# Kernel optimization log

Measured on AMD Instinct MI355X. Metric: run time of the kernel, lower is better.

Reference implementation:

```python
import jax, jax.numpy as jnp
import numpy as np

B, C, M, N = 8, 256, 4, 2048
CK = C // M  # k_conv input channels
EPS_BN = 1e-5


def setup_inputs() -> dict:
    key = jax.random.key(0)
    ks = jax.random.split(key, 10)
    s = 0.05
    return {
        "q": jax.random.normal(ks[0], (B, C, N), jnp.float32),
        "x": jax.random.normal(ks[1], (B, CK, N), jnp.float32),
        "Wq": jax.random.normal(ks[2], (C, C), jnp.float32) * s,   # q_conv (no bias)
        "Wk": jax.random.normal(ks[3], (C, CK), jnp.float32) * s,  # k_conv (no bias)
        "Wv": jax.random.normal(ks[4], (C, C), jnp.float32) * s,   # v_conv
        "bv": jax.random.normal(ks[5], (C,), jnp.float32) * s,
        "Wt": jax.random.normal(ks[6], (C, C), jnp.float32) * s,   # trans_conv
        "bt": jax.random.normal(ks[7], (C,), jnp.float32) * s,
        "gamma": jnp.ones((C,), jnp.float32),                      # BatchNorm1d weight
        "beta": jnp.zeros((C,), jnp.float32),                      # BatchNorm1d bias
    }


def reference(q, x, Wq, Wk, Wv, bv, Wt, bt, gamma, beta):
    # 1x1 Conv1d == per-point channel matmul
    x_q = jnp.einsum("oc,bcn->bno", Wq, q)                  # [B, N, C]
    x_k = jnp.einsum("oc,bcn->bon", Wk, x)                  # [B, C, N]
    x_v = jnp.einsum("oc,bcn->bon", Wv, q) + bv[None, :, None]  # [B, C, N]

    energy = jnp.einsum("bnc,bcm->bnm", x_q, x_k)           # [B, Nq, Nk]
    attention = jax.nn.softmax(energy, axis=-1)
    # extra L1 renormalization over the query dimension (dim=1)
    attention = attention / (1e-9 + attention.sum(axis=1, keepdims=True))

    x_r = jnp.einsum("bcn,bnm->bcm", x_v, attention)        # [B, C, Nk]

    y = jnp.einsum("oc,bcn->bon", Wt, x_r) + bt[None, :, None]
    # BatchNorm1d in training mode: batch statistics over (B, N) per channel
    mean = y.mean(axis=(0, 2), keepdims=True)
    var = ((y - mean) ** 2).mean(axis=(0, 2), keepdims=True)
    y = (y - mean) * jax.lax.rsqrt(var + EPS_BN)
    y = y * gamma[None, :, None] + beta[None, :, None]
    return jax.nn.relu(y)
```

## Files before the change

kernel.cpp:

```cpp
#include <hip/hip_runtime.h>
#include <hip/hip_bf16.h>

#define NB  8
#define NC  256
#define NCK 64
#define SEQ 2048

typedef unsigned short u16;
typedef short bfrag8 __attribute__((ext_vector_type(8)));
typedef float ffrag4 __attribute__((ext_vector_type(4)));

#define MFMA16(a, b, c) __builtin_amdgcn_mfma_f32_16x16x32_bf16((a), (b), (c), 0, 0, 0)

static __device__ __forceinline__ u16 f2bf(float f) {
  return __builtin_bit_cast(u16, (__bf16)f);
}
static __device__ __forceinline__ float bf2f(u16 u) {
  unsigned v = (unsigned)u << 16;
  return __builtin_bit_cast(float, v);
}

__global__ __launch_bounds__(256) void wconv_kernel(
    const float* __restrict__ Wv, const float* __restrict__ Wt,
    u16* __restrict__ dst, float* __restrict__ zz, float* __restrict__ rowsum_g) {
  int bx = blockIdx.x;
  if (bx >= 512) {
    if (bx == 512) {
      zz[threadIdx.x] = 0.f;
      zz[256 + threadIdx.x] = 0.f;
    } else {
      rowsum_g[(bx - 513) * 256 + threadIdx.x] = 0.f;
    }
    return;
  }
  int id = bx * 256 + threadIdx.x;
  const float* src;
  int off;
  if (id < 65536) { src = Wv; off = 131072; }
  else            { src = Wt; off = 262144; id -= 65536; }
  float v = src[id];
  u16 h = f2bf(v);
  u16 l = f2bf(v - bf2f(h));
  dst[off + id] = h;
  dst[off + 65536 + id] = l;
}

template <int CIN>
__global__ __launch_bounds__(256) void tconv_kernel(
    const float* __restrict__ in, u16* __restrict__ Thi, u16* __restrict__ Tlo) {
  __shared__ float t[32][33];
  const int tid = threadIdx.x;
  const int b = blockIdx.x & 7, cg = blockIdx.x >> 3;
  const int c0 = cg << 5, n0 = blockIdx.y << 5;
  {
    int c = tid >> 3, m4 = (tid & 7) << 2;
    float4 v = *(const float4*)&in[((size_t)b * CIN + c0 + c) * SEQ + n0 + m4];
    t[c][m4 + 0] = v.x; t[c][m4 + 1] = v.y; t[c][m4 + 2] = v.z; t[c][m4 + 3] = v.w;
  }
  __syncthreads();
  {
    int n = tid >> 3, c4 = (tid & 7) << 2;
    u16 h[4], l[4];
#pragma unroll
    for (int j = 0; j < 4; ++j) {
      float v = t[c4 + j][n];
      h[j] = f2bf(v);
      l[j] = f2bf(v - bf2f(h[j]));
    }
    size_t base = ((size_t)b * SEQ + n0 + n) * CIN + c0 + c4;
    *(uint2*)&Thi[base] = make_uint2((unsigned)h[0] | ((unsigned)h[1] << 16),
                                     (unsigned)h[2] | ((unsigned)h[3] << 16));
    *(uint2*)&Tlo[base] = make_uint2((unsigned)l[0] | ((unsigned)l[1] << 16),
                                     (unsigned)l[2] | ((unsigned)l[3] << 16));
  }
}

__global__ __launch_bounds__(256) void gcomp_kernel(
    const float* __restrict__ Wq, const float* __restrict__ Wk,
    u16* __restrict__ Gh, u16* __restrict__ Gl) {
  const int ck = blockIdx.x, c = threadIdx.x;
  float s = 0.f;
#pragma unroll 8
  for (int o = 0; o < 256; ++o) s += Wq[o * 256 + c] * Wk[o * 64 + ck];
  u16 h = f2bf(s);
  Gh[ck * 256 + c] = h;
  Gl[ck * 256 + c] = f2bf(s - bf2f(h));
}

template <int K, bool WA>
__global__ __launch_bounds__(256, 2) void gemm_kernel(
    const u16* __restrict__ Ahi, const u16* __restrict__ Alo,
    const u16* __restrict__ Whi, const u16* __restrict__ Wlo,
    const float* __restrict__ bias, u16* __restrict__ outp) {
  constexpr int SP = K + 8;
  extern __shared__ u16 lds[];
  const int tid = threadIdx.x;
  const int wv = tid >> 6, lane = tid & 63, quad = lane >> 4, ln = lane & 15;
  const int b = blockIdx.x & 7, nt = blockIdx.x >> 3;
  const int o0 = blockIdx.y << 6, n0 = nt << 7;

  constexpr int RW = K / 8;
  for (int i = tid; i < 64 * RW; i += 256) {
    int row = i / RW, kc = (i % RW) * 8;
    *(uint4*)&lds[row * SP + kc] = *(const uint4*)&Whi[(size_t)(o0 + row) * K + kc];
    *(uint4*)&lds[(64 + row) * SP + kc] = *(const uint4*)&Wlo[(size_t)(o0 + row) * K + kc];
  }
  constexpr int NA = K / 32;
  bfrag8 ahi[2][NA], alo[2][NA];
#pragma unroll
  for (int rs = 0; rs < 2; ++rs) {
    const u16* ap = Ahi + ((size_t)b * SEQ + n0 + wv * 32 + rs * 16 + ln) * K + quad * 8;
    const u16* al = Alo + ((size_t)b * SEQ + n0 + wv * 32 + rs * 16 + ln) * K + quad * 8;
#pragma unroll
    for (int a = 0; a < NA; ++a) {
      ahi[rs][a] = *(const bfrag8*)(ap + a * 32);
      alo[rs][a] = *(const bfrag8*)(al + a * 32);
    }
  }
  __syncthreads();

  ffrag4 acc[2][4];
#pragma unroll
  for (int ot = 0; ot < 4; ++ot) {
    ffrag4 e0 = {0.f, 0.f, 0.f, 0.f}, e1 = {0.f, 0.f, 0.f, 0.f};
#pragma unroll
    for (int a = 0; a < NA; ++a) {
      bfrag8 wh = *(const bfrag8*)&lds[(ot * 16 + ln) * SP + a * 32 + quad * 8];
      bfrag8 wl = *(const bfrag8*)&lds[(64 + ot * 16 + ln) * SP + a * 32 + quad * 8];
      if (WA) {
        e0 = MFMA16(wh, ahi[0][a], e0);
        e0 = MFMA16(wh, alo[0][a], e0);
        e0 = MFMA16(wl, ahi[0][a], e0);
        e1 = MFMA16(wh, ahi[1][a], e1);
        e1 = MFMA16(wh, alo[1][a], e1);
        e1 = MFMA16(wl, ahi[1][a], e1);
      } else {
        e0 = MFMA16(ahi[0][a], wh, e0);
        e0 = MFMA16(alo[0][a], wh, e0);
        e0 = MFMA16(ahi[0][a], wl, e0);
        e1 = MFMA16(ahi[1][a], wh, e1);
        e1 = MFMA16(alo[1][a], wh, e1);
        e1 = MFMA16(ahi[1][a], wl, e1);
      }
    }
    acc[0][ot] = e0;
    acc[1][ot] = e1;
  }
  __syncthreads();

  if (!WA) {
    u16* tl = lds;
#pragma unroll
    for (int rs = 0; rs < 2; ++rs)
#pragma unroll
      for (int ot = 0; ot < 4; ++ot)
#pragma unroll
        for (int r = 0; r < 4; ++r)
          tl[(wv * 32 + rs * 16 + quad * 4 + r) * 72 + ot * 16 + ln] = f2bf(acc[rs][ot][r]);
    __syncthreads();
    for (int i = tid; i < 128 * 8; i += 256) {
      int row = i >> 3, c8 = (i & 7) * 8;
      *(uint4*)&outp[((size_t)b * SEQ + n0 + row) * NC + o0 + c8] = *(uint4*)&tl[row * 72 + c8];
    }
  } else {
    u16* tl = lds;
#pragma unroll
    for (int rs = 0; rs < 2; ++rs)
#pragma unroll
      for (int ot = 0; ot < 4; ++ot)
#pragma unroll
        for (int r = 0; r < 4; ++r)
          tl[(ot * 16 + quad * 4 + r) * 136 + wv * 32 + rs * 16 + ln] = f2bf(acc[rs][ot][r]);
    __syncthreads();
    for (int i = tid; i < 64 * 16; i += 256) {
      int row = i >> 4, n8 = (i & 15) * 8;
      float bb = (bias != nullptr) ? bias[o0 + row] : 0.f;
      u16 pk[8];
#pragma unroll
      for (int j = 0; j < 8; ++j) pk[j] = f2bf(bf2f(tl[row * 136 + n8 + j]) + bb);
      *(uint4*)&outp[((size_t)b * NC + o0 + row) * SEQ + n0 + n8] = *(uint4*)pk;
    }
  }
}

__global__ __launch_bounds__(256, 2) void gemmxg_kernel(
    const u16* __restrict__ Ahi, const u16* __restrict__ Alo,
    const u16* __restrict__ Gh, const u16* __restrict__ Gl,
    u16* __restrict__ xg) {
  constexpr int K = 256, SP = K + 8;
  __shared__ u16 lds[128 * SP];
  const int tid = threadIdx.x;
  const int wv = tid >> 6, lane = tid & 63, quad = lane >> 4, ln = lane & 15;
  const int b = blockIdx.x & 7, nt = blockIdx.x >> 3;
  const int n0 = nt << 7;

  for (int i = tid; i < 64 * 32; i += 256) {
    int row = i >> 5, kc = (i & 31) * 8;
    *(uint4*)&lds[row * SP + kc] = *(const uint4*)&Gh[(size_t)row * K + kc];
    *(uint4*)&lds[(64 + row) * SP + kc] = *(const uint4*)&Gl[(size_t)row * K + kc];
  }
  bfrag8 ahi[2][8], alo[2][8];
#pragma unroll
  for (int rs = 0; rs < 2; ++rs) {
    const u16* ap = Ahi + ((size_t)b * SEQ + n0 + wv * 32 + rs * 16 + ln) * K + quad * 8;
    const u16* al = Alo + ((size_t)b * SEQ + n0 + wv * 32 + rs * 16 + ln) * K + quad * 8;
#pragma unroll
    for (int a = 0; a < 8; ++a) {
      ahi[rs][a] = *(const bfrag8*)(ap + a * 32);
      alo[rs][a] = *(const bfrag8*)(al + a * 32);
    }
  }
  __syncthreads();

  ffrag4 acc[2][4];
#pragma unroll
  for (int ot = 0; ot < 4; ++ot) {
    ffrag4 e0 = {0.f, 0.f, 0.f, 0.f}, e1 = {0.f, 0.f, 0.f, 0.f};
#pragma unroll
    for (int a = 0; a < 8; ++a) {
      bfrag8 wh = *(const bfrag8*)&lds[(ot * 16 + ln) * SP + a * 32 + quad * 8];
      bfrag8 wl = *(const bfrag8*)&lds[(64 + ot * 16 + ln) * SP + a * 32 + quad * 8];
      e0 = MFMA16(ahi[0][a], wh, e0);
      e0 = MFMA16(alo[0][a], wh, e0);
      e0 = MFMA16(ahi[0][a], wl, e0);
      e1 = MFMA16(ahi[1][a], wh, e1);
      e1 = MFMA16(alo[1][a], wh, e1);
      e1 = MFMA16(ahi[1][a], wl, e1);
    }
    acc[0][ot] = e0;
    acc[1][ot] = e1;
  }
  __syncthreads();

  u16* tl = lds;
#pragma unroll
  for (int rs = 0; rs < 2; ++rs)
#pragma unroll
    for (int ot = 0; ot < 4; ++ot)
#pragma unroll
      for (int r = 0; r < 4; ++r)
        tl[(wv * 32 + rs * 16 + quad * 4 + r) * 72 + ot * 16 + ln] = f2bf(acc[rs][ot][r]);
  __syncthreads();
  for (int i = tid; i < 128 * 8; i += 256) {
    int row = i >> 3, c8 = (i & 7) * 8;
    *(uint4*)&xg[((size_t)b * SEQ + n0 + row) * NCK + c8] = *(uint4*)&tl[row * 72 + c8];
  }
}

__global__ __launch_bounds__(256, 2) void rowsum_kernel(
    const u16* __restrict__ xg, const u16* __restrict__ xTh,
    const u16* __restrict__ xTl, float* __restrict__ rowsum_g) {
  __shared__ u16 bk_l[2][2][64 * 76];
  const int tid = threadIdx.x;
  const int wv = tid >> 6, lane = tid & 63, quad = lane >> 4, ln = lane & 15;
  const int b  = blockIdx.x & 7;
  const int nt = (blockIdx.x >> 3) & 15;
  const int mh = blockIdx.x >> 7;
  const int n0 = nt << 7;
  const int m0 = mh << 9;

  bfrag8 aq[2][2];
#pragma unroll
  for (int rs = 0; rs < 2; ++rs) {
    const u16* qp = xg + ((size_t)b * SEQ + n0 + wv * 32 + rs * 16 + ln) * NCK + quad * 8;
    aq[rs][0] = *(const bfrag8*)qp;
    aq[rs][1] = *(const bfrag8*)(qp + 32);
  }

  const int srow = tid >> 2, scol = (tid & 3) << 4;
  uint4 ph0, ph1, pl0, pl1;
  {
    size_t base = ((size_t)b * SEQ + m0 + srow) * NCK + scol;
    ph0 = *(const uint4*)&xTh[base];     ph1 = *(const uint4*)&xTh[base + 8];
    pl0 = *(const uint4*)&xTl[base];     pl1 = *(const uint4*)&xTl[base + 8];
  }

  float rsum[2][4];
#pragma unroll
  for (int rs = 0; rs < 2; ++rs)
#pragma unroll
    for (int r = 0; r < 4; ++r) rsum[rs][r] = 0.f;

  for (int ch = 0; ch < 8; ++ch) {
    u16* bh = &bk_l[ch & 1][0][srow * 76 + scol];
    u16* bl = &bk_l[ch & 1][1][srow * 76 + scol];
    *(uint4*)bh = ph0; *(uint4*)(bh + 8) = ph1;
    *(uint4*)bl = pl0; *(uint4*)(bl + 8) = pl1;
    if (ch < 7) {
      size_t base = ((size_t)b * SEQ + m0 + (ch + 1) * 64 + srow) * NCK + scol;
      ph0 = *(const uint4*)&xTh[base];   ph1 = *(const uint4*)&xTh[base + 8];
      pl0 = *(const uint4*)&xTl[base];   pl1 = *(const uint4*)&xTl[base + 8];
    }
    __syncthreads();

    ffrag4 e[2][4];
#pragma unroll
    for (int rs = 0; rs < 2; ++rs)
#pragma unroll
      for (int ms = 0; ms < 4; ++ms) e[rs][ms] = (ffrag4){0.f, 0.f, 0.f, 0.f};
#pragma unroll
    for (int ms = 0; ms < 4; ++ms)
#pragma unroll
      for (int kk = 0; kk < 2; ++kk) {
        bfrag8 bbh = *(const bfrag8*)&bk_l[ch & 1][0][(ms * 16 + ln) * 76 + kk * 32 + quad * 8];
        bfrag8 bbl = *(const bfrag8*)&bk_l[ch & 1][1][(ms * 16 + ln) * 76 + kk * 32 + quad * 8];
        e[0][ms] = MFMA16(aq[0][kk], bbh, e[0][ms]);
        e[0][ms] = MFMA16(aq[0][kk], bbl, e[0][ms]);
        e[1][ms] = MFMA16(aq[1][kk], bbh, e[1][ms]);
        e[1][ms] = MFMA16(aq[1][kk], bbl, e[1][ms]);
      }
#pragma unroll
    for (int rs = 0; rs < 2; ++rs)
#pragma unroll
      for (int ms = 0; ms < 4; ++ms)
#pragma unroll
        for (int r = 0; r < 4; ++r) rsum[rs][r] += __expf(e[rs][ms][r]);
  }

#pragma unroll
  for (int msk = 1; msk < 16; msk <<= 1)
#pragma unroll
    for (int rs = 0; rs < 2; ++rs)
#pragma unroll
      for (int r = 0; r < 4; ++r) rsum[rs][r] += __shfl_xor(rsum[rs][r], msk, 64);
  if (ln == 0) {
#pragma unroll
    for (int rs = 0; rs < 2; ++rs)
#pragma unroll
      for (int r = 0; r < 4; ++r)
        atomicAdd(&rowsum_g[(size_t)b * SEQ + n0 + wv * 32 + rs * 16 + quad * 4 + r],
                  rsum[rs][r]);
  }
}

__global__ __launch_bounds__(512, 4) void attn_kernel(
    const u16* __restrict__ xg, const u16* __restrict__ xTh,
    const u16* __restrict__ xTl, const u16* __restrict__ xv,
    const float* __restrict__ rowsum_g,
    u16* __restrict__ U, float* __restrict__ csum) {
  __shared__ u16 xg_l[32 * 76];
  __shared__ u16 p_l[64 * 40];
  __shared__ float ri_l[32];
  __shared__ float cs_l[64];
  const int tid = threadIdx.x;
  const int wv = tid >> 6, lane = tid & 63, quad = lane >> 4, ln = lane & 15;
  const int b = blockIdx.x & 7;
  const int m0 = ((blockIdx.x >> 3) & 31) << 6;
  const int half = blockIdx.x >> 8;
  const int nsub = wv & 1, msub = wv >> 1;
  const int nt0 = half * 32, ntEnd = nt0 + 32;

  if (tid < 64) cs_l[tid] = 0.f;

  bfrag8 bkh[2], bkl[2];
  {
    size_t base = ((size_t)b * SEQ + m0 + msub * 16 + ln) * NCK + quad * 8;
#pragma unroll
    for (int kk = 0; kk < 2; ++kk) {
      bkh[kk] = *(const bfrag8*)&xTh[base + kk * 32];
      bkl[kk] = *(const bfrag8*)&xTl[base + kk * 32];
    }
  }

  const int prow = (tid & 255) >> 3, pcol = (tid & 7) << 3;
  uint4 pf0 = {0, 0, 0, 0};
  float rspf = 1.f;
  bfrag8 avpf0, avpf1;
  {
    const int n0 = nt0 << 5;
    if (tid < 256) pf0 = *(const uint4*)&xg[((size_t)b * SEQ + n0 + prow) * NCK + pcol];
    if (tid < 32) rspf = rowsum_g[(size_t)b * SEQ + n0 + tid];
    const u16* vp = &xv[((size_t)b * NC + wv * 32 + ln) * SEQ + n0 + quad * 8];
    avpf0 = *(const bfrag8*)vp;
    avpf1 = *(const bfrag8*)(vp + 16 * SEQ);
  }

  ffrag4 acc[2][4];
#pragma unroll
  for (int ct = 0; ct < 2; ++ct)
#pragma unroll
    for (int s = 0; s < 4; ++s) acc[ct][s] = (ffrag4){0.f, 0.f, 0.f, 0.f};
  float cs = 0.f;

  for (int nt = nt0; nt < ntEnd; ++nt) {
    bfrag8 av0 = avpf0, av1 = avpf1;
    if (tid < 256) *(uint4*)&xg_l[prow * 76 + pcol] = pf0;
    if (tid < 32) ri_l[tid] = 1.0f / rspf;
    {
      const int ntn = (nt + 1 < ntEnd) ? nt + 1 : nt;
      const int n0n = ntn << 5;
      if (tid < 256) pf0 = *(const uint4*)&xg[((size_t)b * SEQ + n0n + prow) * NCK + pcol];
      if (tid < 32) rspf = rowsum_g[(size_t)b * SEQ + n0n + tid];
      const u16* vp = &xv[((size_t)b * NC + wv * 32 + ln) * SEQ + n0n + quad * 8];
      avpf0 = *(const bfrag8*)vp;
      avpf1 = *(const bfrag8*)(vp + 16 * SEQ);
    }
    __syncthreads();
    {
      ffrag4 e = {0.f, 0.f, 0.f, 0.f};
#pragma unroll
      for (int kk = 0; kk < 2; ++kk) {
        bfrag8 a = *(const bfrag8*)&xg_l[(nsub * 16 + ln) * 76 + kk * 32 + quad * 8];
        e = MFMA16(a, bkh[kk], e);
        e = MFMA16(a, bkl[kk], e);
      }
      u16 pu[4];
#pragma unroll
      for (int r = 0; r < 4; ++r) {
        float p = __expf(e[r]) * ri_l[nsub * 16 + quad * 4 + r];
        cs += p;
        pu[r] = f2bf(p);
      }
      *(uint2*)&p_l[(msub * 16 + ln) * 40 + nsub * 16 + quad * 4] =
          make_uint2((unsigned)pu[0] | ((unsigned)pu[1] << 16),
                     (unsigned)pu[2] | ((unsigned)pu[3] << 16));
    }
    __syncthreads();
#pragma unroll
    for (int s = 0; s < 4; ++s) {
      bfrag8 pb = *(const bfrag8*)&p_l[(s * 16 + ln) * 40 + quad * 8];
      acc[0][s] = MFMA16(av0, pb, acc[0][s]);
      acc[1][s] = MFMA16(av1, pb, acc[1][s]);
    }
  }

  cs += __shfl_down(cs, 32, 64);
  cs += __shfl_down(cs, 16, 64);
  if (lane < 16) atomicAdd(&cs_l[msub * 16 + ln], cs);
  __syncthreads();
  if (tid < 64) csum[((size_t)half * NB + b) * SEQ + m0 + tid] = cs_l[tid];

  u16* Uh = U + (size_t)half * NB * SEQ * NC;
#pragma unroll
  for (int ct = 0; ct < 2; ++ct)
#pragma unroll
    for (int s = 0; s < 4; ++s) {
      u16 pk[4];
#pragma unroll
      for (int r = 0; r < 4; ++r) pk[r] = f2bf(acc[ct][s][r]);
      *(uint2*)&Uh[((size_t)b * SEQ + m0 + s * 16 + ln) * NC + wv * 32 + ct * 16 + quad * 4] =
          make_uint2((unsigned)pk[0] | ((unsigned)pk[1] << 16),
                     (unsigned)pk[2] | ((unsigned)pk[3] << 16));
    }
}

__global__ __launch_bounds__(256, 2) void gemmt_kernel(
    const u16* __restrict__ U, const float* __restrict__ csum,
    const u16* __restrict__ Whi, const u16* __restrict__ Wlo,
    const float* __restrict__ bias, float* __restrict__ outp,
    float* __restrict__ ssum, float* __restrict__ sqsum) {
  constexpr int K = NC, SP = K + 8;
  __shared__ u16 lds[128 * SP];
  __shared__ float bsum[64], bsq[64];
  const int tid = threadIdx.x;
  const int wv = tid >> 6, lane = tid & 63, quad = lane >> 4, ln = lane & 15;
  const int b = blockIdx.x & 7, nt = blockIdx.x >> 3;
  const int o0 = blockIdx.y << 6, n0 = nt << 7;
  const size_t SZu = (size_t)NB * SEQ * NC;

  if (tid < 64) { bsum[tid] = 0.f; bsq[tid] = 0.f; }

  for (int i = tid; i < 64 * 32; i += 256) {
    int row = i >> 5, kc = (i & 31) * 8;
    *(uint4*)&lds[row * SP + kc] = *(const uint4*)&Whi[(size_t)(o0 + row) * K + kc];
    *(uint4*)&lds[(64 + row) * SP + kc] = *(const uint4*)&Wlo[(size_t)(o0 + row) * K + kc];
  }

  bfrag8 af[2][8];
#pragma unroll
  for (int rs = 0; rs < 2; ++rs) {
    const int row = n0 + wv * 32 + rs * 16 + ln;
    const float ic = 1.0f / (1e-9f + csum[(size_t)b * SEQ + row] +
                             csum[((size_t)NB + b) * SEQ + row]);
    const u16* up = U + ((size_t)b * SEQ + row) * NC + quad * 8;
#pragma unroll
    for (int a = 0; a < 8; ++a) {
      bfrag8 u0 = *(const bfrag8*)(up + a * 32);
      bfrag8 u1 = *(const bfrag8*)(up + SZu + a * 32);
      union { u16 u[8]; bfrag8 f; } t;
#pragma unroll
      for (int j = 0; j < 8; ++j)
        t.u[j] = f2bf((bf2f((u16)u0[j]) + bf2f((u16)u1[j])) * ic);
      af[rs][a] = t.f;
    }
  }
  __syncthreads();

  ffrag4 acc[2][4];
#pragma unroll
  for (int ot = 0; ot < 4; ++ot) {
    ffrag4 e0 = {0.f, 0.f, 0.f, 0.f}, e1 = {0.f, 0.f, 0.f, 0.f};
#pragma unroll
    for (int a = 0; a < 8; ++a) {
      bfrag8 wh = *(const bfrag8*)&lds[(ot * 16 + ln) * SP + a * 32 + quad * 8];
      bfrag8 wl = *(const bfrag8*)&lds[(64 + ot * 16 + ln) * SP + a * 32 + quad * 8];
      e0 = MFMA16(wh, af[0][a], e0);
      e0 = MFMA16(wl, af[0][a], e0);
      e1 = MFMA16(wh, af[1][a], e1);
      e1 = MFMA16(wl, af[1][a], e1);
    }
    acc[0][ot] = e0;
    acc[1][ot] = e1;
  }
  __syncthreads();

  float* fl = (float*)lds;
#pragma unroll
  for (int rs = 0; rs < 2; ++rs)
#pragma unroll
    for (int ot = 0; ot < 4; ++ot)
#pragma unroll
      for (int r = 0; r < 4; ++r)
        fl[(ot * 16 + quad * 4 + r) * 132 + wv * 32 + rs * 16 + ln] = acc[rs][ot][r];
  __syncthreads();
  for (int i = tid; i < 64 * 32; i += 256) {
    int row = i >> 5, n4 = (i & 31) * 4;
    float bb = (bias != nullptr) ? bias[o0 + row] : 0.f;
    const float* src = &fl[row * 132 + n4];
    float4 v = *(const float4*)src;
    v.x += bb; v.y += bb; v.z += bb; v.w += bb;
    *(float4*)&outp[((size_t)b * NC + o0 + row) * SEQ + n0 + n4] = v;
    float s = v.x + v.y + v.z + v.w;
    float sq = v.x * v.x + v.y * v.y + v.z * v.z + v.w * v.w;
    atomicAdd(&bsum[row], s);
    atomicAdd(&bsq[row], sq);
  }
  __syncthreads();
  if (tid < 64) {
    atomicAdd(&ssum[o0 + tid], bsum[tid]);
    atomicAdd(&sqsum[o0 + tid], bsq[tid]);
  }
}

__global__ __launch_bounds__(256) void bnorm_kernel(
    const float* __restrict__ y, const float* __restrict__ ssum, const float* __restrict__ sqsum,
    const float* __restrict__ gamma, const float* __restrict__ beta, float* __restrict__ out) {
  size_t e0 = ((size_t)blockIdx.x * 256 + threadIdx.x) * 4;
  int o = (int)((e0 >> 11) & (NC - 1));
  const float invn = 1.0f / 16384.0f;
  float mean = ssum[o] * invn;
  float var = sqsum[o] * invn - mean * mean;
  float rs = rsqrtf(var + 1e-5f);
  float a = gamma[o] * rs;
  float c = beta[o] - mean * a;
  float4 v = *(const float4*)(y + e0);
  float4 r;
  r.x = fmaxf(0.f, fmaf(v.x, a, c));
  r.y = fmaxf(0.f, fmaf(v.y, a, c));
  r.z = fmaxf(0.f, fmaf(v.z, a, c));
  r.w = fmaxf(0.f, fmaf(v.w, a, c));
  *(float4*)(out + e0) = r;
}

extern "C" void kernel_launch(void* const* d_in, const int* in_sizes, int n_in,
                              void* d_out, int out_size, void* d_ws, size_t ws_size,
                              hipStream_t stream) {
  const float* q     = (const float*)d_in[0];
  const float* x     = (const float*)d_in[1];
  const float* Wq    = (const float*)d_in[2];
  const float* Wk    = (const float*)d_in[3];
  const float* Wv    = (const float*)d_in[4];
  const float* bv    = (const float*)d_in[5];
  const float* Wt    = (const float*)d_in[6];
  const float* bt    = (const float*)d_in[7];
  const float* gamma = (const float*)d_in[8];
  const float* beta  = (const float*)d_in[9];
  float* out = (float*)d_out;

  const size_t SZ = (size_t)NB * NC * SEQ;
  const size_t SZB = SZ * 4;
  char* wsb = (char*)d_ws;
  u16* qT_hi = (u16*)(wsb);
  u16* qT_lo = qT_hi + SZ;
  u16* U     = (u16*)(wsb);
  float* y   = (float*)(wsb + 2 * SZB);
  u16* xv    = (u16*)(wsb + 3 * SZB);
  u16* wpack = (u16*)(wsb + 3 * SZB + SZB / 2);
  u16* Wv_hi = wpack + 131072, *Wv_lo = wpack + 196608;
  u16* Wt_hi = wpack + 262144, *Wt_lo = wpack + 327680;
  float* rowsum_g = (float*)(wpack + 425984);
  float* csum = rowsum_g + (size_t)NB * SEQ;
  float* ssum = csum + 2 * (size_t)NB * SEQ;
  float* sqsum = ssum + NC;
  u16* xT_hi = (u16*)(wsb + ((size_t)64 << 20));
  u16* xT_lo = (u16*)(wsb + ((size_t)66 << 20));
  u16* xg    = (u16*)(wsb + ((size_t)72 << 20));
  u16* Gp_hi = (u16*)(wsb + ((size_t)78 << 20));
  u16* Gp_lo = Gp_hi + 64 * 256;

  wconv_kernel<<<577, 256, 0, stream>>>(Wv, Wt, wpack, ssum, rowsum_g);
  tconv_kernel<NC><<<dim3(64, 64), 256, 0, stream>>>(q, qT_hi, qT_lo);
  tconv_kernel<NCK><<<dim3(16, 64), 256, 0, stream>>>(x, xT_hi, xT_lo);
  gcomp_kernel<<<64, 256, 0, stream>>>(Wq, Wk, Gp_hi, Gp_lo);

  const size_t shm256 = 64 * (256 + 8) * 2 * sizeof(u16);
  gemm_kernel<256, true><<<dim3(128, 4), 256, shm256, stream>>>(
      qT_hi, qT_lo, Wv_hi, Wv_lo, bv, xv);
  gemmxg_kernel<<<128, 256, 0, stream>>>(qT_hi, qT_lo, Gp_hi, Gp_lo, xg);

  rowsum_kernel<<<512, 256, 0, stream>>>(xg, xT_hi, xT_lo, rowsum_g);
  attn_kernel<<<512, 512, 0, stream>>>(xg, xT_hi, xT_lo, xv, rowsum_g, U, csum);
  gemmt_kernel<<<dim3(128, 4), 256, 0, stream>>>(
      U, csum, Wt_hi, Wt_lo, bt, y, ssum, sqsum);

  bnorm_kernel<<<4096, 256, 0, stream>>>(y, ssum, sqsum, gamma, beta, out);
}
```

Measured before the change: 224.2 us.

## Split attention and rowsum over more blocks, load fragments directly from global

The rowsum and attention kernels are split four ways along their reduction dimension instead of two, doubling the grid to 1024 blocks. Attention partials now go to two U buffers with four csum slices that the Wt GEMM sums. Both kernels drop the LDS staging of xg and key tiles and load MFMA fragments straight from global memory. Attention double-buffers the probability tile so each iteration needs one barrier instead of two. This targets low occupancy and barrier overhead, at the cost of writing and reading twice as much partial-U traffic in the GEMM.

```diff
diff --git a/kernel.cpp b/kernel.cpp
--- a/kernel.cpp
+++ b/kernel.cpp
@@ -250,14 +250,13 @@
 __global__ __launch_bounds__(256, 2) void rowsum_kernel(
     const u16* __restrict__ xg, const u16* __restrict__ xTh,
     const u16* __restrict__ xTl, float* __restrict__ rowsum_g) {
-  __shared__ u16 bk_l[2][2][64 * 76];
   const int tid = threadIdx.x;
   const int wv = tid >> 6, lane = tid & 63, quad = lane >> 4, ln = lane & 15;
   const int b  = blockIdx.x & 7;
   const int nt = (blockIdx.x >> 3) & 15;
   const int mh = blockIdx.x >> 7;
   const int n0 = nt << 7;
-  const int m0 = mh << 9;
+  const int m0 = mh << 8;
 
   bfrag8 aq[2][2];
 #pragma unroll
@@ -267,32 +266,25 @@
     aq[rs][1] = *(const bfrag8*)(qp + 32);
   }
 
-  const int srow = tid >> 2, scol = (tid & 3) << 4;
-  uint4 ph0, ph1, pl0, pl1;
-  {
-    size_t base = ((size_t)b * SEQ + m0 + srow) * NCK + scol;
-    ph0 = *(const uint4*)&xTh[base];     ph1 = *(const uint4*)&xTh[base + 8];
-    pl0 = *(const uint4*)&xTl[base];     pl1 = *(const uint4*)&xTl[base + 8];
-  }
-
   float rsum[2][4];
 #pragma unroll
   for (int rs = 0; rs < 2; ++rs)
 #pragma unroll
     for (int r = 0; r < 4; ++r) rsum[rs][r] = 0.f;
 
-  for (int ch = 0; ch < 8; ++ch) {
-    u16* bh = &bk_l[ch & 1][0][srow * 76 + scol];
-    u16* bl = &bk_l[ch & 1][1][srow * 76 + scol];
-    *(uint4*)bh = ph0; *(uint4*)(bh + 8) = ph1;
-    *(uint4*)bl = pl0; *(uint4*)(bl + 8) = pl1;
-    if (ch < 7) {
-      size_t base = ((size_t)b * SEQ + m0 + (ch + 1) * 64 + srow) * NCK + scol;
-      ph0 = *(const uint4*)&xTh[base];   ph1 = *(const uint4*)&xTh[base + 8];
-      pl0 = *(const uint4*)&xTl[base];   pl1 = *(const uint4*)&xTl[base + 8];
-    }
-    __syncthreads();
-
+  const size_t kbase = ((size_t)b * SEQ + m0 + ln) * NCK + quad * 8;
+
+#pragma unroll
+  for (int ch = 0; ch < 4; ++ch) {
+    bfrag8 bh[4][2], bl[4][2];
+#pragma unroll
+    for (int ms = 0; ms < 4; ++ms) {
+      size_t base = kbase + (size_t)(ch * 64 + ms * 16) * NCK;
+      bh[ms][0] = *(const bfrag8*)&xTh[base];
+      bh[ms][1] = *(const bfrag8*)&xTh[base + 32];
+      bl[ms][0] = *(const bfrag8*)&xTl[base];
+      bl[ms][1] = *(const bfrag8*)&xTl[base + 32];
+    }
     ffrag4 e[2][4];
 #pragma unroll
     for (int rs = 0; rs < 2; ++rs)
@@ -302,12 +294,10 @@
     for (int ms = 0; ms < 4; ++ms)
 #pragma unroll
       for (int kk = 0; kk < 2; ++kk) {
-        bfrag8 bbh = *(const bfrag8*)&bk_l[ch & 1][0][(ms * 16 + ln) * 76 + kk * 32 + quad * 8];
-        bfrag8 bbl = *(const bfrag8*)&bk_l[ch & 1][1][(ms * 16 + ln) * 76 + kk * 32 + quad * 8];
-        e[0][ms] = MFMA16(aq[0][kk], bbh, e[0][ms]);
-        e[0][ms] = MFMA16(aq[0][kk], bbl, e[0][ms]);
-        e[1][ms] = MFMA16(aq[1][kk], bbh, e[1][ms]);
-        e[1][ms] = MFMA16(aq[1][kk], bbl, e[1][ms]);
+        e[0][ms] = MFMA16(aq[0][kk], bh[ms][kk], e[0][ms]);
+        e[0][ms] = MFMA16(aq[0][kk], bl[ms][kk], e[0][ms]);
+        e[1][ms] = MFMA16(aq[1][kk], bh[ms][kk], e[1][ms]);
+        e[1][ms] = MFMA16(aq[1][kk], bl[ms][kk], e[1][ms]);
       }
 #pragma unroll
     for (int rs = 0; rs < 2; ++rs)
@@ -337,43 +327,38 @@
     const u16* __restrict__ xg, const u16* __restrict__ xTh,
     const u16* __restrict__ xTl, const u16* __restrict__ xv,
     const float* __restrict__ rowsum_g,
-    u16* __restrict__ U, float* __restrict__ csum) {
-  __shared__ u16 xg_l[32 * 76];
-  __shared__ u16 p_l[64 * 40];
-  __shared__ float ri_l[32];
+    u16* __restrict__ Ua, u16* __restrict__ Ub, float* __restrict__ csum) {
+  __shared__ u16 p_l[2][64 * 40];
   __shared__ float cs_l[64];
   const int tid = threadIdx.x;
   const int wv = tid >> 6, lane = tid & 63, quad = lane >> 4, ln = lane & 15;
   const int b = blockIdx.x & 7;
   const int m0 = ((blockIdx.x >> 3) & 31) << 6;
-  const int half = blockIdx.x >> 8;
+  const int qtr = blockIdx.x >> 8;
   const int nsub = wv & 1, msub = wv >> 1;
-  const int nt0 = half * 32, ntEnd = nt0 + 32;
+  const int nt0 = qtr * 16, ntEnd = nt0 + 16;
 
   if (tid < 64) cs_l[tid] = 0.f;
 
-  bfrag8 bkh[2], bkl[2];
+  bfrag8 bkh0, bkh1, bkl0, bkl1;
   {
     size_t base = ((size_t)b * SEQ + m0 + msub * 16 + ln) * NCK + quad * 8;
-#pragma unroll
-    for (int kk = 0; kk < 2; ++kk) {
-      bkh[kk] = *(const bfrag8*)&xTh[base + kk * 32];
-      bkl[kk] = *(const bfrag8*)&xTl[base + kk * 32];
-    }
-  }
-
-  const int prow = (tid & 255) >> 3, pcol = (tid & 7) << 3;
-  uint4 pf0 = {0, 0, 0, 0};
-  float rspf = 1.f;
-  bfrag8 avpf0, avpf1;
-  {
-    const int n0 = nt0 << 5;
-    if (tid < 256) pf0 = *(const uint4*)&xg[((size_t)b * SEQ + n0 + prow) * NCK + pcol];
-    if (tid < 32) rspf = rowsum_g[(size_t)b * SEQ + n0 + tid];
-    const u16* vp = &xv[((size_t)b * NC + wv * 32 + ln) * SEQ + n0 + quad * 8];
-    avpf0 = *(const bfrag8*)vp;
-    avpf1 = *(const bfrag8*)(vp + 16 * SEQ);
-  }
+    bkh0 = *(const bfrag8*)&xTh[base];
+    bkh1 = *(const bfrag8*)&xTh[base + 32];
+    bkl0 = *(const bfrag8*)&xTl[base];
+    bkl1 = *(const bfrag8*)&xTl[base + 32];
+  }
+
+  const size_t aoff = ((size_t)b * SEQ + nsub * 16 + ln) * NCK + quad * 8;
+  const size_t voff = ((size_t)b * NC + wv * 32 + ln) * SEQ + quad * 8;
+  const size_t roff = (size_t)b * SEQ + nsub * 16 + quad * 4;
+
+  int n0 = nt0 << 5;
+  bfrag8 a0 = *(const bfrag8*)&xg[aoff + (size_t)n0 * NCK];
+  bfrag8 a1 = *(const bfrag8*)&xg[aoff + (size_t)n0 * NCK + 32];
+  bfrag8 av0 = *(const bfrag8*)&xv[voff + n0];
+  bfrag8 av1 = *(const bfrag8*)&xv[voff + n0 + 16 * SEQ];
+  float4 rsv = *(const float4*)&rowsum_g[roff + n0];
 
   ffrag4 acc[2][4];
 #pragma unroll
@@ -381,56 +366,56 @@
 #pragma unroll
     for (int s = 0; s < 4; ++s) acc[ct][s] = (ffrag4){0.f, 0.f, 0.f, 0.f};
   float cs = 0.f;
+  int buf = 0;
 
   for (int nt = nt0; nt < ntEnd; ++nt) {
-    bfrag8 av0 = avpf0, av1 = avpf1;
-    if (tid < 256) *(uint4*)&xg_l[prow * 76 + pcol] = pf0;
-    if (tid < 32) ri_l[tid] = 1.0f / rspf;
+    {
+      ffrag4 e = {0.f, 0.f, 0.f, 0.f};
+      e = MFMA16(a0, bkh0, e);
+      e = MFMA16(a0, bkl0, e);
+      e = MFMA16(a1, bkh1, e);
+      e = MFMA16(a1, bkl1, e);
+      u16 pu[4];
+#pragma unroll
+      for (int r = 0; r < 4; ++r) {
+        float p = __expf(e[r]) * (1.0f / ((r == 0) ? rsv.x : (r == 1) ? rsv.y : (r == 2) ? rsv.z : rsv.w));
+        cs += p;
+        pu[r] = f2bf(p);
+      }
+      *(uint2*)&p_l[buf][(msub * 16 + ln) * 40 + nsub * 16 + quad * 4] =
+          make_uint2((unsigned)pu[0] | ((unsigned)pu[1] << 16),
+                     (unsigned)pu[2] | ((unsigned)pu[3] << 16));
+    }
+    bfrag8 a0n, a1n, av0n, av1n;
+    float4 rsvn;
     {
       const int ntn = (nt + 1 < ntEnd) ? nt + 1 : nt;
       const int n0n = ntn << 5;
-      if (tid < 256) pf0 = *(const uint4*)&xg[((size_t)b * SEQ + n0n + prow) * NCK + pcol];
-      if (tid < 32) rspf = rowsum_g[(size_t)b * SEQ + n0n + tid];
-      const u16* vp = &xv[((size_t)b * NC + wv * 32 + ln) * SEQ + n0n + quad * 8];
-      avpf0 = *(const bfrag8*)vp;
-      avpf1 = *(const bfrag8*)(vp + 16 * SEQ);
+      a0n = *(const bfrag8*)&xg[aoff + (size_t)n0n * NCK];
+      a1n = *(const bfrag8*)&xg[aoff + (size_t)n0n * NCK + 32];
+      av0n = *(const bfrag8*)&xv[voff + n0n];
+      av1n = *(const bfrag8*)&xv[voff + n0n + 16 * SEQ];
+      rsvn = *(const float4*)&rowsum_g[roff + n0n];
     }
     __syncthreads();
-    {
-      ffrag4 e = {0.f, 0.f, 0.f, 0.f};
-#pragma unroll
-      for (int kk = 0; kk < 2; ++kk) {
-        bfrag8 a = *(const bfrag8*)&xg_l[(nsub * 16 + ln) * 76 + kk * 32 + quad * 8];
-        e = MFMA16(a, bkh[kk], e);
-        e = MFMA16(a, bkl[kk], e);
-      }
-      u16 pu[4];
-#pragma unroll
-      for (int r = 0; r < 4; ++r) {
-        float p = __expf(e[r]) * ri_l[nsub * 16 + quad * 4 + r];
-        cs += p;
-        pu[r] = f2bf(p);
-      }
-      *(uint2*)&p_l[(msub * 16 + ln) * 40 + nsub * 16 + quad * 4] =
-          make_uint2((unsigned)pu[0] | ((unsigned)pu[1] << 16),
-                     (unsigned)pu[2] | ((unsigned)pu[3] << 16));
-    }
-    __syncthreads();
 #pragma unroll
     for (int s = 0; s < 4; ++s) {
-      bfrag8 pb = *(const bfrag8*)&p_l[(s * 16 + ln) * 40 + quad * 8];
+      bfrag8 pb = *(const bfrag8*)&p_l[buf][(s * 16 + ln) * 40 + quad * 8];
       acc[0][s] = MFMA16(av0, pb, acc[0][s]);
       acc[1][s] = MFMA16(av1, pb, acc[1][s]);
     }
+    a0 = a0n; a1 = a1n; av0 = av0n; av1 = av1n; rsv = rsvn;
+    buf ^= 1;
   }
 
   cs += __shfl_down(cs, 32, 64);
   cs += __shfl_down(cs, 16, 64);
   if (lane < 16) atomicAdd(&cs_l[msub * 16 + ln], cs);
   __syncthreads();
-  if (tid < 64) csum[((size_t)half * NB + b) * SEQ + m0 + tid] = cs_l[tid];
-
-  u16* Uh = U + (size_t)half * NB * SEQ * NC;
+  if (tid < 64) csum[((size_t)qtr * NB + b) * SEQ + m0 + tid] = cs_l[tid];
+
+  const size_t SZu = (size_t)NB * SEQ * NC;
+  u16* Uh = ((qtr < 2) ? Ua : Ub) + (size_t)(qtr & 1) * SZu;
 #pragma unroll
   for (int ct = 0; ct < 2; ++ct)
 #pragma unroll
@@ -445,7 +430,8 @@
 }
 
 __global__ __launch_bounds__(256, 2) void gemmt_kernel(
-    const u16* __restrict__ U, const float* __restrict__ csum,
+    const u16* __restrict__ Ua, const u16* __restrict__ Ub,
+    const float* __restrict__ csum,
     const u16* __restrict__ Whi, const u16* __restrict__ Wlo,
     const float* __restrict__ bias, float* __restrict__ outp,
     float* __restrict__ ssum, float* __restrict__ sqsum) {
@@ -470,17 +456,24 @@
 #pragma unroll
   for (int rs = 0; rs < 2; ++rs) {
     const int row = n0 + wv * 32 + rs * 16 + ln;
-    const float ic = 1.0f / (1e-9f + csum[(size_t)b * SEQ + row] +
-                             csum[((size_t)NB + b) * SEQ + row]);
-    const u16* up = U + ((size_t)b * SEQ + row) * NC + quad * 8;
+    const float ic = 1.0f / (1e-9f +
+                             csum[(size_t)b * SEQ + row] +
+                             csum[((size_t)NB + b) * SEQ + row] +
+                             csum[((size_t)2 * NB + b) * SEQ + row] +
+                             csum[((size_t)3 * NB + b) * SEQ + row]);
+    const u16* up0 = Ua + ((size_t)b * SEQ + row) * NC + quad * 8;
+    const u16* up1 = Ub + ((size_t)b * SEQ + row) * NC + quad * 8;
 #pragma unroll
     for (int a = 0; a < 8; ++a) {
-      bfrag8 u0 = *(const bfrag8*)(up + a * 32);
-      bfrag8 u1 = *(const bfrag8*)(up + SZu + a * 32);
+      bfrag8 u0 = *(const bfrag8*)(up0 + a * 32);
+      bfrag8 u1 = *(const bfrag8*)(up0 + SZu + a * 32);
+      bfrag8 u2 = *(const bfrag8*)(up1 + a * 32);
+      bfrag8 u3 = *(const bfrag8*)(up1 + SZu + a * 32);
       union { u16 u[8]; bfrag8 f; } t;
 #pragma unroll
       for (int j = 0; j < 8; ++j)
-        t.u[j] = f2bf((bf2f((u16)u0[j]) + bf2f((u16)u1[j])) * ic);
+        t.u[j] = f2bf((bf2f((u16)u0[j]) + bf2f((u16)u1[j]) +
+                       bf2f((u16)u2[j]) + bf2f((u16)u3[j])) * ic);
       af[rs][a] = t.f;
     }
   }
@@ -572,7 +565,7 @@
   char* wsb = (char*)d_ws;
   u16* qT_hi = (u16*)(wsb);
   u16* qT_lo = qT_hi + SZ;
-  u16* U     = (u16*)(wsb);
+  u16* Ua    = (u16*)(wsb);
   float* y   = (float*)(wsb + 2 * SZB);
   u16* xv    = (u16*)(wsb + 3 * SZB);
   u16* wpack = (u16*)(wsb + 3 * SZB + SZB / 2);
@@ -580,13 +573,14 @@
   u16* Wt_hi = wpack + 262144, *Wt_lo = wpack + 327680;
   float* rowsum_g = (float*)(wpack + 425984);
   float* csum = rowsum_g + (size_t)NB * SEQ;
-  float* ssum = csum + 2 * (size_t)NB * SEQ;
+  float* ssum = csum + 4 * (size_t)NB * SEQ;
   float* sqsum = ssum + NC;
   u16* xT_hi = (u16*)(wsb + ((size_t)64 << 20));
   u16* xT_lo = (u16*)(wsb + ((size_t)66 << 20));
   u16* xg    = (u16*)(wsb + ((size_t)72 << 20));
   u16* Gp_hi = (u16*)(wsb + ((size_t)78 << 20));
   u16* Gp_lo = Gp_hi + 64 * 256;
+  u16* Ub    = (u16*)(wsb + ((size_t)80 << 20));
 
   wconv_kernel<<<577, 256, 0, stream>>>(Wv, Wt, wpack, ssum, rowsum_g);
   tconv_kernel<NC><<<dim3(64, 64), 256, 0, stream>>>(q, qT_hi, qT_lo);
@@ -598,10 +592,10 @@
       qT_hi, qT_lo, Wv_hi, Wv_lo, bv, xv);
   gemmxg_kernel<<<128, 256, 0, stream>>>(qT_hi, qT_lo, Gp_hi, Gp_lo, xg);
 
-  rowsum_kernel<<<512, 256, 0, stream>>>(xg, xT_hi, xT_lo, rowsum_g);
-  attn_kernel<<<512, 512, 0, stream>>>(xg, xT_hi, xT_lo, xv, rowsum_g, U, csum);
+  rowsum_kernel<<<1024, 256, 0, stream>>>(xg, xT_hi, xT_lo, rowsum_g);
+  attn_kernel<<<1024, 512, 0, stream>>>(xg, xT_hi, xT_lo, xv, rowsum_g, Ua, Ub, csum);
   gemmt_kernel<<<dim3(128, 4), 256, 0, stream>>>(
-      U, csum, Wt_hi, Wt_lo, bt, y, ssum, sqsum);
+      Ua, Ub, csum, Wt_hi, Wt_lo, bt, y, ssum, sqsum);
 
   bnorm_kernel<<<4096, 256, 0, stream>>>(y, ssum, sqsum, gamma, beta, out);
 }
```

Result: slower. 276.3 us (+23.2%).
